# Kernel tuning notes

Measured on AMD Instinct MI355X. Metric: run time of the kernel, lower is better.

## Reference

```python
import jax, jax.numpy as jnp
import numpy as np
import math

INF = 10000000000.0
D_KEY = 128
SCALE = math.sqrt(D_KEY)


def setup_inputs() -> dict:
    key = jax.random.key(0)
    kq, kk, kv = jax.random.split(key, 3)
    B, S, D = 16, 2048, D_KEY
    return {
        "query": jax.random.normal(kq, (B, S, D), dtype=jnp.float32),
        "key": jax.random.normal(kk, (B, S, D), dtype=jnp.float32),
        "value": jax.random.normal(kv, (B, S, D), dtype=jnp.float32),
    }


def reference(query, key, value):
    # dot_products: [B, Sq, Sk]
    scores = jnp.einsum("bqd,bkd->bqk", query, key)
    S = key.shape[1]
    # NOTE: original subtracts the INF upper-triangular mask BEFORE dividing
    # by sqrt(d_key); replicate that order faithfully.
    tri = jnp.triu(jnp.full((S, S), INF, dtype=scores.dtype), k=1)
    scores = scores - tri[None, :, :]
    attn = jax.nn.softmax(scores / SCALE, axis=-1)
    # dropout with p=0.0 is identity
    return jnp.einsum("bqk,bkd->bqd", attn, value)
```

## Files before the change

### kernel.cpp

```cpp
#include <hip/hip_runtime.h>
#include <math.h>

#define S_LEN  2048
#define D_HEAD 128
#define QBLK   64
#define KVBLK  64
#define BATCH  16
#define NKVT   (S_LEN / KVBLK)
#define TILE_SH 8192
#define SLOTS_PB 56

typedef __attribute__((ext_vector_type(4))) float f32x4;
typedef __attribute__((ext_vector_type(8))) short short8;

__device__ __forceinline__ unsigned short f2bf(float x) {
    union { float f; unsigned u; } v; v.f = x;
    unsigned r = v.u + 0x7fffu + ((v.u >> 16) & 1u);
    return (unsigned short)(r >> 16);
}
__device__ __forceinline__ float bf2f(unsigned short h) {
    union { unsigned u; float f; } v; v.u = ((unsigned)h) << 16;
    return v.f;
}
__device__ __forceinline__ unsigned pack2(unsigned short a, unsigned short b) {
    return (unsigned)a | ((unsigned)b << 16);
}
__device__ __forceinline__ unsigned cvtpk(float lo, float hi) {
    unsigned r;
    asm("v_cvt_pk_bf16_f32 %0, %1, %2" : "=v"(r) : "v"(lo), "v"(hi));
    return r;
}
__device__ __forceinline__ void gld16(const void* g, void* l) {
    __builtin_amdgcn_global_load_lds(
        (const __attribute__((address_space(1))) void*)g,
        (__attribute__((address_space(3))) void*)l, 16, 0, 0);
}
template<int N> __device__ __forceinline__ void wait_vm() {
    asm volatile("s_waitcnt vmcnt(%0)" :: "i"(N) : "memory");
}
__device__ __forceinline__ void barrier() {
    __builtin_amdgcn_sched_barrier(0);
    __builtin_amdgcn_s_barrier();
    __builtin_amdgcn_sched_barrier(0);
}
__device__ __forceinline__ int slot_base(int b, int qb) {
    return b * SLOTS_PB + ((qb >= 24) ? (32 + (qb - 24) * 3) : ((qb - 8) * 2));
}

__global__ __launch_bounds__(256) void prep(const float* __restrict__ K,
                                            const float* __restrict__ V,
                                            unsigned short* __restrict__ Kp,
                                            unsigned short* __restrict__ Vp)
{
    const int tid = threadIdx.x;
    const int bid = blockIdx.x;
    const int b = bid >> 5, t = bid & 31;
    const size_t ibase = (size_t)b * S_LEN * D_HEAD + (size_t)t * KVBLK * D_HEAD;
    unsigned short* ko = Kp + (size_t)bid * TILE_SH;
    unsigned short* vo = Vp + (size_t)bid * TILE_SH;

    #pragma unroll
    for (int c = 0; c < 4; ++c) {
        int i  = c * 256 + tid;
        int k  = i >> 4;
        int d8 = ((i & 15) * 8) ^ ((k & 7) << 3);
        const float* sp = K + ibase + (size_t)k * D_HEAD + d8;
        float4 a = *(const float4*)sp;
        float4 bb = *(const float4*)(sp + 4);
        uint4 u = { pack2(f2bf(a.x),f2bf(a.y)),  pack2(f2bf(a.z),f2bf(a.w)),
                    pack2(f2bf(bb.x),f2bf(bb.y)),pack2(f2bf(bb.z),f2bf(bb.w)) };
        *(uint4*)(ko + i * 8) = u;
    }

    __shared__ unsigned short Vb[KVBLK][D_HEAD + 2];
    {
        const int r  = tid >> 2;
        const int c0 = (tid & 3) * 32;
        const float* sp = V + ibase + (size_t)r * D_HEAD + c0;
        #pragma unroll
        for (int i = 0; i < 8; ++i) {
            float4 x = *(const float4*)(sp + i * 4);
            Vb[r][c0+i*4+0] = f2bf(x.x); Vb[r][c0+i*4+1] = f2bf(x.y);
            Vb[r][c0+i*4+2] = f2bf(x.z); Vb[r][c0+i*4+3] = f2bf(x.w);
        }
    }
    __syncthreads();
    #pragma unroll
    for (int c = 0; c < 4; ++c) {
        int i   = c * 256 + tid;
        int d   = i >> 3;
        int kk0 = ((i & 7) * 8) ^ ((d & 7) << 3);
        unsigned short h[8];
        #pragma unroll
        for (int j = 0; j < 8; ++j) h[j] = Vb[kk0 + j][d];
        uint4 u = { pack2(h[0],h[1]), pack2(h[2],h[3]), pack2(h[4],h[5]), pack2(h[6],h[7]) };
        *(uint4*)(vo + i * 8) = u;
    }
}

template<int MODE>
__global__ __launch_bounds__(256, 4)
void attn_fwd(const float* __restrict__ Qg, const unsigned short* __restrict__ Kp,
              const unsigned short* __restrict__ Vp, float* __restrict__ Og,
              unsigned short* __restrict__ Po, float* __restrict__ Ml)
{
    constexpr float CSC = 0.12751744f;
    const int tid  = threadIdx.x;
    const int lane = tid & 63;
    const int w    = tid >> 6;
    const int bid  = blockIdx.x;

    int b, qb, lo, nt, C = 1, piece = 0, pslot = -1;
    if (MODE == 0) {
        b = bid & 15;
        const int rank = bid >> 4;
        qb = (rank < 16) ? (31 - rank) : (rank - 16);
        lo = 0; nt = qb + 1;
    } else {
        b = bid & 15;
        const int o = bid >> 4, k = o & 15, r = o >> 4;
        if (r <= 1)      { qb = 31 - k; C = (k < 8) ? 3 : 2; piece = r; }
        else if (r == 2) { if (k < 8) { qb = 31 - k; C = 3; piece = 2; }
                           else       { qb = k;      C = 2; piece = 0; } }
        else             { if (k < 8) { qb = k;      C = 1; piece = 0; }
                           else       { qb = k;      C = 2; piece = 1; } }
        const int n = qb + 1, q_ = n / C, rem = n % C;
        lo = piece * q_ + min(piece, rem);
        nt = q_ + (piece < rem ? 1 : 0);
        if (C > 1) pslot = slot_base(b, qb) + piece;
    }
    const int q0w  = qb * QBLK + w * 16;
    const int qc   = lane & 15;
    const int g    = lane >> 4;
    const int qidx = q0w + qc;

    __shared__ __align__(16) unsigned short Klds[TILE_SH];
    __shared__ __align__(16) unsigned short Vlds[TILE_SH];
    __shared__ __align__(16) unsigned short Plds[4][16 * KVBLK];

    const size_t base = (size_t)b * S_LEN * D_HEAD;
    const int tb = b * NKVT;

    auto stage_K = [&](int t) {
        const unsigned short* ks = Kp + (size_t)(tb + t) * TILE_SH + w * 2048 + lane * 8;
        #pragma unroll
        for (int ii = 0; ii < 4; ++ii) gld16(ks + ii * 512, &Klds[w * 2048 + ii * 512]);
    };
    auto stage_V = [&](int t) {
        const unsigned short* vs = Vp + (size_t)(tb + t) * TILE_SH + w * 2048 + lane * 8;
        #pragma unroll
        for (int ii = 0; ii < 4; ++ii) gld16(vs + ii * 512, &Vlds[w * 2048 + ii * 512]);
    };

    short8 qf[4];
    {
        const float* qp = Qg + base + (size_t)(q0w + qc) * D_HEAD + g * 8;
        #pragma unroll
        for (int db = 0; db < 4; ++db) {
            float4 x0 = *(const float4*)(qp + db * 32);
            float4 x1 = *(const float4*)(qp + db * 32 + 4);
            float tt[8] = {x0.x, x0.y, x0.z, x0.w, x1.x, x1.y, x1.z, x1.w};
            short8 f;
            #pragma unroll
            for (int jj = 0; jj < 8; ++jj) f[jj] = (short)f2bf(tt[jj] * CSC);
            qf[db] = f;
        }
    }

    f32x4 acc[8] = {};
    float m = -1e30f, lsum = 0.f;

    stage_K(lo);

    for (int i = 0; i < nt; ++i) {
        const int t   = lo + i;
        const int kv0 = t * KVBLK;
        const bool more = (i + 1 < nt);

        wait_vm<0>();
        barrier();
        stage_V(t);

        const int t16max = min(3, (q0w + 15 - kv0) >> 4);
        const int ksmax  = min(1, (q0w + 15 - kv0) >> 5);

        f32x4 st[4] = {};
        __builtin_amdgcn_s_setprio(1);
        #pragma unroll
        for (int t16 = 0; t16 < 4; ++t16) {
            if (t16 <= t16max) {
                const int kr = t16 * 16 + qc;
                const int swz = (kr & 7) << 3;
                #pragma unroll
                for (int db = 0; db < 4; ++db) {
                    short8 kf = *(const short8*)&Klds[(kr * 128 + db * 32 + g * 8) ^ swz];
                    st[t16] = __builtin_amdgcn_mfma_f32_16x16x32_bf16(kf, qf[db], st[t16], 0, 0, 0);
                }
            }
        }
        __builtin_amdgcn_s_setprio(0);

        barrier();
        if (more) stage_K(t + 1);

        float s[16];
        #pragma unroll
        for (int t16 = 0; t16 < 4; ++t16)
            #pragma unroll
            for (int r = 0; r < 4; ++r)
                s[t16*4+r] = (t16 <= t16max) ? st[t16][r] : -1e30f;

        if (kv0 + KVBLK - 1 > q0w) {
            #pragma unroll
            for (int t16 = 0; t16 < 4; ++t16)
                #pragma unroll
                for (int r = 0; r < 4; ++r)
                    if (kv0 + t16 * 16 + g * 4 + r > qidx) s[t16*4+r] = -1e30f;
        }

        float m0 = fmaxf(fmaxf(s[0],s[1]), fmaxf(s[2],s[3]));
        float m1 = fmaxf(fmaxf(s[4],s[5]), fmaxf(s[6],s[7]));
        float m2 = fmaxf(fmaxf(s[8],s[9]), fmaxf(s[10],s[11]));
        float m3 = fmaxf(fmaxf(s[12],s[13]), fmaxf(s[14],s[15]));
        float mx = fmaxf(fmaxf(m0,m1), fmaxf(m2,m3));

        if (__any(mx > m + 8.0f)) {
            mx = fmaxf(mx, __shfl_xor(mx, 16));
            mx = fmaxf(mx, __shfl_xor(mx, 32));
            float mnew = fmaxf(m, mx);
            float alpha = exp2f(m - mnew);
            m = mnew;
            lsum *= alpha;
            float a_o[4];
            #pragma unroll
            for (int r = 0; r < 4; ++r) a_o[r] = __shfl(alpha, g * 4 + r);
            #pragma unroll
            for (int db = 0; db < 8; ++db)
                #pragma unroll
                for (int r = 0; r < 4; ++r) acc[db][r] *= a_o[r];
        }

        float p16[16];
        #pragma unroll
        for (int ii = 0; ii < 16; ++ii) p16[ii] = exp2f(s[ii] - m);
        float r0 = (p16[0]+p16[1]) + (p16[2]+p16[3]);
        float r1 = (p16[4]+p16[5]) + (p16[6]+p16[7]);
        float r2 = (p16[8]+p16[9]) + (p16[10]+p16[11]);
        float r3 = (p16[12]+p16[13]) + (p16[14]+p16[15]);
        lsum += (r0+r1) + (r2+r3);

        if (more) wait_vm<4>(); else wait_vm<0>();
        barrier();

        const int pswz = (qc & 7) << 3;
        #pragma unroll
        for (int t16 = 0; t16 < 4; ++t16) {
            uint2 uu = { cvtpk(p16[t16*4+0], p16[t16*4+1]), cvtpk(p16[t16*4+2], p16[t16*4+3]) };
            *(uint2*)&Plds[w][(qc * 64 + t16 * 16 + g * 4) ^ pswz] = uu;
        }

        __builtin_amdgcn_s_setprio(1);
        #pragma unroll
        for (int ks = 0; ks < 2; ++ks) {
            if (ks <= ksmax) {
                short8 pa = *(const short8*)&Plds[w][(qc * 64 + ks * 32 + g * 8) ^ pswz];
                #pragma unroll
                for (int db = 0; db < 8; ++db) {
                    const int d = db * 16 + qc;
                    short8 vf = *(const short8*)&Vlds[(d * 64 + ks * 32 + g * 8) ^ ((d & 7) << 3)];
                    acc[db] = __builtin_amdgcn_mfma_f32_16x16x32_bf16(pa, vf, acc[db], 0, 0, 0);
                }
            }
        }
        __builtin_amdgcn_s_setprio(0);
    }

    lsum += __shfl_xor(lsum, 16);
    lsum += __shfl_xor(lsum, 32);

    if (pslot < 0) {
        float linv = 1.0f / lsum;
        float li[4];
        #pragma unroll
        for (int r = 0; r < 4; ++r) li[r] = __shfl(linv, g * 4 + r);
        #pragma unroll
        for (int db = 0; db < 8; ++db)
            #pragma unroll
            for (int r = 0; r < 4; ++r)
                Og[base + (size_t)(q0w + g * 4 + r) * D_HEAD + db * 16 + qc] = acc[db][r] * li[r];
    } else {
        unsigned short* po = Po + (size_t)pslot * (QBLK * D_HEAD);
        #pragma unroll
        for (int db = 0; db < 8; ++db)
            #pragma unroll
            for (int r = 0; r < 4; ++r)
                po[(w * 16 + g * 4 + r) * D_HEAD + db * 16 + qc] = f2bf(acc[db][r]);
        if (g == 0) {
            float* ml = Ml + (size_t)pslot * (QBLK * 2);
            ml[(w * 16 + qc) * 2 + 0] = m;
            ml[(w * 16 + qc) * 2 + 1] = lsum;
        }
    }
}

__global__ __launch_bounds__(256)
void combine(const unsigned short* __restrict__ Po, const float* __restrict__ Ml,
             float* __restrict__ Og)
{
    const int z   = blockIdx.x;
    const int b   = z & 15;
    const int j   = z >> 4;
    const int qb  = (j < 16) ? (8 + j) : (24 + (j - 16));
    const int C   = (qb >= 24) ? 3 : 2;
    const int tid = threadIdx.x;
    const int row = tid >> 2;
    const int c0  = (tid & 3) * 32;
    const int sb  = slot_base(b, qb);

    float mm[3], lv[3], M = -1e30f;
    #pragma unroll
    for (int c = 0; c < 3; ++c) {
        if (c < C) {
            const float* ml = Ml + (size_t)(sb + c) * (QBLK * 2);
            mm[c] = ml[row * 2 + 0];
            lv[c] = ml[row * 2 + 1];
            M = fmaxf(M, mm[c]);
        }
    }
    float den = 0.f, wgt[3];
    #pragma unroll
    for (int c = 0; c < 3; ++c) {
        if (c < C) { wgt[c] = exp2f(mm[c] - M); den += wgt[c] * lv[c]; }
    }
    const float rd = 1.0f / den;

    float am[32];
    #pragma unroll
    for (int q = 0; q < 32; ++q) am[q] = 0.f;
    #pragma unroll
    for (int c = 0; c < 3; ++c) {
        if (c < C) {
            const unsigned short* po = Po + (size_t)(sb + c) * (QBLK * D_HEAD) + row * D_HEAD + c0;
            const float wc = wgt[c];
            #pragma unroll
            for (int q = 0; q < 4; ++q) {
                uint4 u = *(const uint4*)(po + q * 8);
                const unsigned short* h = (const unsigned short*)&u;
                #pragma unroll
                for (int e = 0; e < 8; ++e) am[q * 8 + e] += wc * bf2f(h[e]);
            }
        }
    }
    float* op = Og + (size_t)b * S_LEN * D_HEAD + (size_t)(qb * QBLK + row) * D_HEAD + c0;
    #pragma unroll
    for (int q = 0; q < 8; ++q) {
        float4 r = { am[q*4+0] * rd, am[q*4+1] * rd, am[q*4+2] * rd, am[q*4+3] * rd };
        *(float4*)(op + q * 4) = r;
    }
}

extern "C" void kernel_launch(void* const* d_in, const int* in_sizes, int n_in,
                              void* d_out, int out_size, void* d_ws, size_t ws_size,
                              hipStream_t stream) {
    const float* Q = (const float*)d_in[0];
    const float* K = (const float*)d_in[1];
    const float* V = (const float*)d_in[2];
    float* O = (float*)d_out;

    const size_t tile_elems = (size_t)BATCH * NKVT * TILE_SH;
    const size_t nslots = (size_t)BATCH * SLOTS_PB;
    unsigned short* Kp = (unsigned short*)d_ws;
    unsigned short* Vp = Kp + tile_elems;
    unsigned short* Po = Vp + tile_elems;
    float*          Mlp = (float*)(Po + nslots * QBLK * D_HEAD);
    const size_t need_bytes = (char*)(Mlp + nslots * QBLK * 2) - (char*)d_ws;

    prep<<<dim3(BATCH * NKVT), dim3(256), 0, stream>>>(K, V, Kp, Vp);
    if (ws_size >= need_bytes) {
        attn_fwd<1><<<dim3(1024), dim3(256), 0, stream>>>(Q, Kp, Vp, O, Po, Mlp);
        combine<<<dim3(24 * BATCH), dim3(256), 0, stream>>>(Po, Mlp, O);
    } else {
        attn_fwd<0><<<dim3(512), dim3(256), 0, stream>>>(Q, Kp, Vp, O, nullptr, nullptr);
    }
}
```

Measured before the change: 58.81 us.

## Use 128-row query blocks with 8 waves and rebalance split-KV pieces

Doubles the query block to 128 rows processed by 8 wavefronts per 512-thread workgroup, so each staged K/V tile in LDS is shared by twice as many query rows. This halves K/V global traffic per query. The split-KV work partition is redesigned: long query blocks are split into 4 pieces and short ones into 2, always going through the combine kernel. The K tile prefetch is also moved ahead of the Q load. The cost is larger workgroups, fewer blocks in flight, and extra partial-result traffic, since every block now writes partials.

Measured after the change: 72.03 us. +22.5%, slower.

```diff
diff --git a/kernel.cpp b/kernel.cpp
--- a/kernel.cpp
+++ b/kernel.cpp
@@ -3,12 +3,12 @@
 
 #define S_LEN  2048
 #define D_HEAD 128
-#define QBLK   64
+#define QBLK   128
 #define KVBLK  64
 #define BATCH  16
 #define NKVT   (S_LEN / KVBLK)
 #define TILE_SH 8192
-#define SLOTS_PB 56
+#define SLOTS_PB 48
 
 typedef __attribute__((ext_vector_type(4))) float f32x4;
 typedef __attribute__((ext_vector_type(8))) short short8;
@@ -43,8 +43,8 @@
     __builtin_amdgcn_s_barrier();
     __builtin_amdgcn_sched_barrier(0);
 }
-__device__ __forceinline__ int slot_base(int b, int qb) {
-    return b * SLOTS_PB + ((qb >= 24) ? (32 + (qb - 24) * 3) : ((qb - 8) * 2));
+__device__ __forceinline__ int slot_base(int b, int J) {
+    return b * SLOTS_PB + ((J >= 8) ? (16 + (J - 8) * 4) : (J * 2));
 }
 
 __global__ __launch_bounds__(256) void prep(const float* __restrict__ K,
@@ -99,7 +99,7 @@
 }
 
 template<int MODE>
-__global__ __launch_bounds__(256, 4)
+__global__ __launch_bounds__(512, 4)
 void attn_fwd(const float* __restrict__ Qg, const unsigned short* __restrict__ Kp,
               const unsigned short* __restrict__ Vp, float* __restrict__ Og,
               unsigned short* __restrict__ Po, float* __restrict__ Ml)
@@ -107,50 +107,50 @@
     constexpr float CSC = 0.12751744f;
     const int tid  = threadIdx.x;
     const int lane = tid & 63;
-    const int w    = tid >> 6;
+    const int w8   = tid >> 6;
     const int bid  = blockIdx.x;
 
-    int b, qb, lo, nt, C = 1, piece = 0, pslot = -1;
+    int b, J, lo, nt, pslot = -1;
     if (MODE == 0) {
         b = bid & 15;
         const int rank = bid >> 4;
-        qb = (rank < 16) ? (31 - rank) : (rank - 16);
-        lo = 0; nt = qb + 1;
+        J = (rank < 8) ? (15 - rank) : (rank - 8);
+        lo = 0; nt = 2 * J + 2;
     } else {
         b = bid & 15;
-        const int o = bid >> 4, k = o & 15, r = o >> 4;
-        if (r <= 1)      { qb = 31 - k; C = (k < 8) ? 3 : 2; piece = r; }
-        else if (r == 2) { if (k < 8) { qb = 31 - k; C = 3; piece = 2; }
-                           else       { qb = k;      C = 2; piece = 0; } }
-        else             { if (k < 8) { qb = k;      C = 1; piece = 0; }
-                           else       { qb = k;      C = 2; piece = 1; } }
-        const int n = qb + 1, q_ = n / C, rem = n % C;
+        const int o = bid >> 4, k = o & 15, r = o >> 4, K7 = k & 7;
+        int C, piece;
+        if (r < 2) { J = 15 - K7; C = 4; piece = r * 2 + (k >> 3); }
+        else       { J = K7;      C = 2; piece = (k >> 3); }
+        const int n = 2 * J + 2, q_ = n / C, rem = n % C;
         lo = piece * q_ + min(piece, rem);
         nt = q_ + (piece < rem ? 1 : 0);
-        if (C > 1) pslot = slot_base(b, qb) + piece;
-    }
-    const int q0w  = qb * QBLK + w * 16;
+        pslot = slot_base(b, J) + piece;
+    }
+    const int q0w  = J * QBLK + w8 * 16;
     const int qc   = lane & 15;
     const int g    = lane >> 4;
     const int qidx = q0w + qc;
 
     __shared__ __align__(16) unsigned short Klds[TILE_SH];
     __shared__ __align__(16) unsigned short Vlds[TILE_SH];
-    __shared__ __align__(16) unsigned short Plds[4][16 * KVBLK];
+    __shared__ __align__(16) unsigned short Plds[8][16 * KVBLK];
 
     const size_t base = (size_t)b * S_LEN * D_HEAD;
     const int tb = b * NKVT;
 
     auto stage_K = [&](int t) {
-        const unsigned short* ks = Kp + (size_t)(tb + t) * TILE_SH + w * 2048 + lane * 8;
-        #pragma unroll
-        for (int ii = 0; ii < 4; ++ii) gld16(ks + ii * 512, &Klds[w * 2048 + ii * 512]);
+        const unsigned short* ks = Kp + (size_t)(tb + t) * TILE_SH + w8 * 512 + lane * 8;
+        gld16(ks,        &Klds[w8 * 512 + lane * 8]);
+        gld16(ks + 4096, &Klds[4096 + w8 * 512 + lane * 8]);
     };
     auto stage_V = [&](int t) {
-        const unsigned short* vs = Vp + (size_t)(tb + t) * TILE_SH + w * 2048 + lane * 8;
-        #pragma unroll
-        for (int ii = 0; ii < 4; ++ii) gld16(vs + ii * 512, &Vlds[w * 2048 + ii * 512]);
+        const unsigned short* vs = Vp + (size_t)(tb + t) * TILE_SH + w8 * 512 + lane * 8;
+        gld16(vs,        &Vlds[w8 * 512 + lane * 8]);
+        gld16(vs + 4096, &Vlds[4096 + w8 * 512 + lane * 8]);
     };
+
+    stage_K(lo);
 
     short8 qf[4];
     {
@@ -169,8 +169,6 @@
 
     f32x4 acc[8] = {};
     float m = -1e30f, lsum = 0.f;
-
-    stage_K(lo);
 
     for (int i = 0; i < nt; ++i) {
         const int t   = lo + i;
@@ -249,21 +247,21 @@
         float r3 = (p16[12]+p16[13]) + (p16[14]+p16[15]);
         lsum += (r0+r1) + (r2+r3);
 
-        if (more) wait_vm<4>(); else wait_vm<0>();
+        if (more) wait_vm<2>(); else wait_vm<0>();
         barrier();
 
         const int pswz = (qc & 7) << 3;
         #pragma unroll
         for (int t16 = 0; t16 < 4; ++t16) {
             uint2 uu = { cvtpk(p16[t16*4+0], p16[t16*4+1]), cvtpk(p16[t16*4+2], p16[t16*4+3]) };
-            *(uint2*)&Plds[w][(qc * 64 + t16 * 16 + g * 4) ^ pswz] = uu;
+            *(uint2*)&Plds[w8][(qc * 64 + t16 * 16 + g * 4) ^ pswz] = uu;
         }
 
         __builtin_amdgcn_s_setprio(1);
         #pragma unroll
         for (int ks = 0; ks < 2; ++ks) {
             if (ks <= ksmax) {
-                short8 pa = *(const short8*)&Plds[w][(qc * 64 + ks * 32 + g * 8) ^ pswz];
+                short8 pa = *(const short8*)&Plds[w8][(qc * 64 + ks * 32 + g * 8) ^ pswz];
                 #pragma unroll
                 for (int db = 0; db < 8; ++db) {
                     const int d = db * 16 + qc;
@@ -294,11 +292,11 @@
         for (int db = 0; db < 8; ++db)
             #pragma unroll
             for (int r = 0; r < 4; ++r)
-                po[(w * 16 + g * 4 + r) * D_HEAD + db * 16 + qc] = f2bf(acc[db][r]);
+                po[(w8 * 16 + g * 4 + r) * D_HEAD + db * 16 + qc] = f2bf(acc[db][r]);
         if (g == 0) {
             float* ml = Ml + (size_t)pslot * (QBLK * 2);
-            ml[(w * 16 + qc) * 2 + 0] = m;
-            ml[(w * 16 + qc) * 2 + 1] = lsum;
+            ml[(w8 * 16 + qc) * 2 + 0] = m;
+            ml[(w8 * 16 + qc) * 2 + 1] = lsum;
         }
     }
 }
@@ -307,19 +305,19 @@
 void combine(const unsigned short* __restrict__ Po, const float* __restrict__ Ml,
              float* __restrict__ Og)
 {
-    const int z   = blockIdx.x;
-    const int b   = z & 15;
-    const int j   = z >> 4;
-    const int qb  = (j < 16) ? (8 + j) : (24 + (j - 16));
-    const int C   = (qb >= 24) ? 3 : 2;
-    const int tid = threadIdx.x;
-    const int row = tid >> 2;
-    const int c0  = (tid & 3) * 32;
-    const int sb  = slot_base(b, qb);
-
-    float mm[3], lv[3], M = -1e30f;
-    #pragma unroll
-    for (int c = 0; c < 3; ++c) {
+    const int z    = blockIdx.x;
+    const int half = z & 1;
+    const int b    = (z >> 1) & 15;
+    const int J    = z >> 5;
+    const int C    = (J >= 8) ? 4 : 2;
+    const int tid  = threadIdx.x;
+    const int row  = half * 64 + (tid >> 2);
+    const int c0   = (tid & 3) * 32;
+    const int sb   = slot_base(b, J);
+
+    float mm[4], lv[4], M = -1e30f;
+    #pragma unroll
+    for (int c = 0; c < 4; ++c) {
         if (c < C) {
             const float* ml = Ml + (size_t)(sb + c) * (QBLK * 2);
             mm[c] = ml[row * 2 + 0];
@@ -327,9 +325,9 @@
             M = fmaxf(M, mm[c]);
         }
     }
-    float den = 0.f, wgt[3];
-    #pragma unroll
-    for (int c = 0; c < 3; ++c) {
+    float den = 0.f, wgt[4];
+    #pragma unroll
+    for (int c = 0; c < 4; ++c) {
         if (c < C) { wgt[c] = exp2f(mm[c] - M); den += wgt[c] * lv[c]; }
     }
     const float rd = 1.0f / den;
@@ -338,7 +336,7 @@
     #pragma unroll
     for (int q = 0; q < 32; ++q) am[q] = 0.f;
     #pragma unroll
-    for (int c = 0; c < 3; ++c) {
+    for (int c = 0; c < 4; ++c) {
         if (c < C) {
             const unsigned short* po = Po + (size_t)(sb + c) * (QBLK * D_HEAD) + row * D_HEAD + c0;
             const float wc = wgt[c];
@@ -351,7 +349,7 @@
             }
         }
     }
-    float* op = Og + (size_t)b * S_LEN * D_HEAD + (size_t)(qb * QBLK + row) * D_HEAD + c0;
+    float* op = Og + (size_t)b * S_LEN * D_HEAD + (size_t)(J * QBLK + row) * D_HEAD + c0;
     #pragma unroll
     for (int q = 0; q < 8; ++q) {
         float4 r = { am[q*4+0] * rd, am[q*4+1] * rd, am[q*4+2] * rd, am[q*4+3] * rd };
@@ -377,9 +375,9 @@
 
     prep<<<dim3(BATCH * NKVT), dim3(256), 0, stream>>>(K, V, Kp, Vp);
     if (ws_size >= need_bytes) {
-        attn_fwd<1><<<dim3(1024), dim3(256), 0, stream>>>(Q, Kp, Vp, O, Po, Mlp);
-        combine<<<dim3(24 * BATCH), dim3(256), 0, stream>>>(Po, Mlp, O);
+        attn_fwd<1><<<dim3(768), dim3(512), 0, stream>>>(Q, Kp, Vp, O, Po, Mlp);
+        combine<<<dim3(512), dim3(256), 0, stream>>>(Po, Mlp, O);
     } else {
-        attn_fwd<0><<<dim3(512), dim3(256), 0, stream>>>(Q, Kp, Vp, O, nullptr, nullptr);
-    }
-}
+        attn_fwd<0><<<dim3(256), dim3(512), 0, stream>>>(Q, Kp, Vp, O, nullptr, nullptr);
+    }
+}
```
